# Kernel tuning notes

Measured on AMD Instinct MI355X. Metric: run time of the kernel, lower is better.

The kernel has to match this reference:

```python
import jax, jax.numpy as jnp
import numpy as np

D_MODEL = 1024
N_HEADS = 16
D_HIDDEN = 4096
BATCH = 2
N_CTX = 2048


def setup_inputs() -> dict:
    key = jax.random.key(0)
    ks = jax.random.split(key, 4)
    scale = 0.02
    x = jax.random.normal(ks[0], (BATCH, N_CTX, D_MODEL), dtype=jnp.float32)
    Wk = jax.random.normal(ks[1], (D_MODEL, D_MODEL), dtype=jnp.float32) * scale
    bk = jnp.zeros((D_MODEL,), dtype=jnp.float32)
    Wv = jax.random.normal(ks[2], (D_MODEL, D_HIDDEN), dtype=jnp.float32) * scale
    bv = jnp.zeros((D_HIDDEN,), dtype=jnp.float32)
    Wf = jax.random.normal(ks[3], (D_HIDDEN, D_MODEL), dtype=jnp.float32) * scale
    bf = jnp.zeros((D_MODEL,), dtype=jnp.float32)
    return {"x": x, "Wk": Wk, "bk": bk, "Wv": Wv, "bv": bv, "Wf": Wf, "bf": bf}


def _split_heads(t, n_heads):
    # [..., S, D] -> [..., H, S, D/H]
    B, S, D = t.shape
    return t.reshape(B, S, n_heads, D // n_heads).transpose(0, 2, 1, 3)


def reference(x, Wk, bk, Wv, bv, Wf, bf):
    B, S, D = x.shape
    H = N_HEADS
    # Q is raw x split into heads (no query projection in this module)
    Q = _split_heads(x, H)                  # [B,H,S,dk]
    K = _split_heads(x @ Wk + bk, H)        # [B,H,S,dk]
    V = _split_heads(x @ Wv + bv, H)        # [B,H,S,dv]
    # additive causal mask: 0 on/below diagonal, -inf strictly above
    causal = jnp.tril(jnp.ones((S, S), dtype=bool))
    mask = jnp.where(causal, 0.0, -jnp.inf).astype(x.dtype)
    # NOTE: no 1/sqrt(d) scaling, faithful to the original
    scores = jnp.einsum("bhqd,bhkd->bhqk", Q, K) + mask
    attn = jax.nn.softmax(scores, axis=-1)
    o = jnp.einsum("bhqk,bhkd->bhqd", attn, V)   # [B,H,S,dv]
    o = o.transpose(0, 2, 1, 3).reshape(B, S, -1)  # [B,S,d_hidden]
    return x + jax.nn.gelu(o, approximate=False) @ Wf + bf
```

## Files before the change

kernel.cpp:

```cpp
#include <hip/hip_runtime.h>
#include <math.h>

typedef unsigned short u16;
typedef __attribute__((ext_vector_type(8))) short bf16x8;
typedef __attribute__((ext_vector_type(4))) float f32x4;

__device__ __forceinline__ float b2f(u16 u) {
    union { unsigned int i; float f; } v; v.i = ((unsigned int)u) << 16; return v.f;
}
__device__ __forceinline__ u16 f2b(float f) {
    union { float f; unsigned int i; } v; v.f = f;
    unsigned int r = v.i + 0x7FFFu + ((v.i >> 16) & 1u);
    return (u16)(r >> 16);
}
__device__ __forceinline__ float gelu_exact(float v) {
    return 0.5f * v * (1.0f + erff(v * 0.70710678118654752f));
}

__device__ __forceinline__ void load_lds16(const u16* gp, u16* lp) {
    __builtin_amdgcn_global_load_lds(
        (const __attribute__((address_space(1))) void*)gp,
        (__attribute__((address_space(3))) void*)lp,
        16, 0, 0);
}

__global__ __launch_bounds__(256) void convert_f2b(const float* __restrict__ in,
                                                   u16* __restrict__ out) {
    const int idx = blockIdx.x * 256 + threadIdx.x;
    float4 v = ((const float4*)in)[idx];
    ushort4 u; u.x = f2b(v.x); u.y = f2b(v.y); u.z = f2b(v.z); u.w = f2b(v.w);
    ((ushort4*)out)[idx] = u;
}

__global__ __launch_bounds__(256) void transpose_w(const float* __restrict__ W,
                                                   u16* __restrict__ Wt, int N, int K) {
    __shared__ float t[32][33];
    const int tid = threadIdx.x;
    const int k0 = blockIdx.y * 32, n0 = blockIdx.x * 32;
    const int c = tid & 31, r = tid >> 5;
    #pragma unroll
    for (int p = 0; p < 4; p++)
        t[r + p * 8][c] = W[(size_t)(k0 + r + p * 8) * N + n0 + c];
    __syncthreads();
    #pragma unroll
    for (int p = 0; p < 4; p++)
        Wt[(size_t)(n0 + r + p * 8) * K + k0 + c] = f2b(t[c][r + p * 8]);
}

__global__ __launch_bounds__(256) void transpose_v(const u16* __restrict__ V,
                                                   u16* __restrict__ Vt) {
    __shared__ u16 t[32][36];
    const int tid = threadIdx.x;
    const int bb = blockIdx.z;
    const int s0 = blockIdx.y * 32, c0 = blockIdx.x * 32;
    const int c = tid & 31, r = tid >> 5;
    #pragma unroll
    for (int p = 0; p < 4; p++)
        t[r + p * 8][c] = V[((size_t)(bb * 2048 + s0 + r + p * 8) << 12) + c0 + c];
    __syncthreads();
    #pragma unroll
    for (int p = 0; p < 4; p++)
        Vt[((size_t)(bb * 4096 + c0 + r + p * 8) << 11) + s0 + c] = t[c][r + p * 8];
}

template <int EPI>
__global__ __launch_bounds__(256) void mfma_gemm(
    const u16* __restrict__ A, const u16* __restrict__ Bt,
    const float* __restrict__ bias, const float* __restrict__ resid,
    void* __restrict__ Cv, int M, int N, int K)
{
    __shared__ u16 As[64 * 64];
    __shared__ u16 Bs[128 * 64];

    const int tid = threadIdx.x;
    const int w = tid >> 6, lane = tid & 63;
    const int m16 = lane & 15, quad = lane >> 4;
    const int wm = w >> 1, wn = w & 1;
    const int row0 = blockIdx.y * 64, col0 = blockIdx.x * 128;
    const int lr = lane >> 3, lc = lane & 7;
    const int sw8 = (lc ^ (lr & 7)) * 8;

    f32x4 acc[2][4];
    #pragma unroll
    for (int i = 0; i < 2; i++)
        #pragma unroll
        for (int j = 0; j < 4; j++) acc[i][j] = (f32x4){0.f, 0.f, 0.f, 0.f};

    for (int k0 = 0; k0 < K; k0 += 64) {
        __syncthreads();
        #pragma unroll
        for (int c2 = 0; c2 < 2; c2++)
            load_lds16(A + (size_t)(row0 + c2 * 32 + w * 8 + lr) * K + k0 + sw8,
                       &As[(c2 * 32 + w * 8) * 64]);
        #pragma unroll
        for (int c2 = 0; c2 < 4; c2++)
            load_lds16(Bt + (size_t)(col0 + c2 * 32 + w * 8 + lr) * K + k0 + sw8,
                       &Bs[(c2 * 32 + w * 8) * 64]);
        __syncthreads();

        bf16x8 af[2][2], bfr[4][2];
        #pragma unroll
        for (int mt = 0; mt < 2; mt++)
            #pragma unroll
            for (int ks = 0; ks < 2; ks++)
                af[mt][ks] = *(const bf16x8*)&As[(wm * 32 + mt * 16 + m16) * 64 +
                                                 (((ks * 4 + quad) ^ (m16 & 7)) * 8)];
        #pragma unroll
        for (int nt = 0; nt < 4; nt++)
            #pragma unroll
            for (int ks = 0; ks < 2; ks++)
                bfr[nt][ks] = *(const bf16x8*)&Bs[(wn * 64 + nt * 16 + m16) * 64 +
                                                  (((ks * 4 + quad) ^ (m16 & 7)) * 8)];

        #pragma unroll
        for (int ks = 0; ks < 2; ks++)
            #pragma unroll
            for (int mt = 0; mt < 2; mt++)
                #pragma unroll
                for (int nt = 0; nt < 4; nt++)
                    acc[mt][nt] = __builtin_amdgcn_mfma_f32_16x16x32_bf16(af[mt][ks], bfr[nt][ks], acc[mt][nt], 0, 0, 0);
    }

    #pragma unroll
    for (int mt = 0; mt < 2; mt++) {
        #pragma unroll
        for (int nt = 0; nt < 4; nt++) {
            const int c = col0 + wn * 64 + nt * 16 + m16;
            const float bc = bias[c];
            #pragma unroll
            for (int reg = 0; reg < 4; reg++) {
                const int r = row0 + wm * 32 + mt * 16 + quad * 4 + reg;
                float v = acc[mt][nt][reg] + bc;
                if (EPI == 1) {
                    v += resid[(size_t)r * N + c];
                    ((float*)Cv)[(size_t)r * N + c] = v;
                } else {
                    ((u16*)Cv)[(size_t)r * N + c] = f2b(v);
                }
            }
        }
    }
}

__global__ __launch_bounds__(256) void attn_kernel(
    const float* __restrict__ X,
    const u16*  __restrict__ Kb,
    const u16*  __restrict__ Vt,
    u16* __restrict__ O,
    int B, int S)
{
    const int DM = 1024, DH = 4096;
    __shared__ u16 Qs[64 * 64];
    __shared__ u16 Ks[64 * 64];
    __shared__ u16 Ps[64 * 64];
    __shared__ u16 Vts[256 * 64];

    const int tid = threadIdx.x;
    const int w = tid >> 6, lane = tid & 63;
    const int m16 = lane & 15, quad = lane >> 4;
    const int lr = lane >> 3, lc = lane & 7;
    const int sw8 = (lc ^ (lr & 7)) * 8;
    const int b = blockIdx.z, h = blockIdx.y;
    const int qt = (S / 64 - 1) - blockIdx.x;
    const int q0 = qt * 64;
    const size_t baseRow = (size_t)b * S;

    #pragma unroll
    for (int pass = 0; pass < 2; pass++) {
        const int row = pass * 32 + w * 8 + lr;
        const float* src = X + (baseRow + q0 + row) * DM + h * 64 + sw8;
        float4 v0 = ((const float4*)src)[0];
        float4 v1 = ((const float4*)src)[1];
        bf16x8 u;
        u[0] = (short)f2b(v0.x); u[1] = (short)f2b(v0.y); u[2] = (short)f2b(v0.z); u[3] = (short)f2b(v0.w);
        u[4] = (short)f2b(v1.x); u[5] = (short)f2b(v1.y); u[6] = (short)f2b(v1.z); u[7] = (short)f2b(v1.w);
        *(bf16x8*)&Qs[(pass * 32 + w * 8) * 64 + lane * 8] = u;
    }

    f32x4 o_acc[16];
    #pragma unroll
    for (int i = 0; i < 16; i++) o_acc[i] = (f32x4){0.f, 0.f, 0.f, 0.f};
    f32x4 lacc = (f32x4){0.f, 0.f, 0.f, 0.f};

    bf16x8 onesf;
    {
        const short one = (m16 == 0) ? (short)0x3F80 : (short)0;
        #pragma unroll
        for (int i = 0; i < 8; i++) onesf[i] = one;
    }

    const int nch = qt + 1;
    for (int ch = 0; ch < nch; ch++) {
        const int k0 = ch * 64;
        __syncthreads();

        #pragma unroll
        for (int pass = 0; pass < 2; pass++) {
            const int row = pass * 32 + w * 8 + lr;
            *(bf16x8*)&Ks[(pass * 32 + w * 8) * 64 + lane * 8] =
                *(const bf16x8*)(Kb + (baseRow + k0 + row) * DM + h * 64 + sw8);
        }
        #pragma unroll
        for (int pass = 0; pass < 8; pass++) {
            const int row = pass * 32 + w * 8 + lr;
            *(bf16x8*)&Vts[(pass * 32 + w * 8) * 64 + lane * 8] =
                *(const bf16x8*)(Vt + (((size_t)((b * 16 + h) * 256 + row)) << 11) + k0 + sw8);
        }
        __syncthreads();

        bf16x8 aq[2];
        #pragma unroll
        for (int ks = 0; ks < 2; ks++)
            aq[ks] = *(const bf16x8*)&Qs[(w * 16 + m16) * 64 + (((ks * 4 + quad) ^ (m16 & 7)) * 8)];
        f32x4 sf[4];
        #pragma unroll
        for (int nt = 0; nt < 4; nt++) {
            f32x4 acc = (f32x4){0.f, 0.f, 0.f, 0.f};
            #pragma unroll
            for (int ks = 0; ks < 2; ks++) {
                bf16x8 bk8 = *(const bf16x8*)&Ks[(nt * 16 + m16) * 64 + (((ks * 4 + quad) ^ (m16 & 7)) * 8)];
                acc = __builtin_amdgcn_mfma_f32_16x16x32_bf16(aq[ks], bk8, acc, 0, 0, 0);
            }
            sf[nt] = acc;
        }

        const int qg = q0 + w * 16 + quad * 4;
        #pragma unroll
        for (int nt = 0; nt < 4; nt++) {
            const int kg = k0 + nt * 16 + m16;
            #pragma unroll
            for (int reg = 0; reg < 4; reg++) {
                const float p = (kg <= qg + reg) ? __expf(sf[nt][reg] - 20.f) : 0.f;
                const int srow = w * 16 + quad * 4 + reg;
                Ps[srow * 64 + (((nt * 2 + (m16 >> 3)) ^ (srow & 7)) * 8) + (m16 & 7)] = f2b(p);
            }
        }

        bf16x8 pa[2];
        #pragma unroll
        for (int ks = 0; ks < 2; ks++)
            pa[ks] = *(const bf16x8*)&Ps[(w * 16 + m16) * 64 + (((ks * 4 + quad) ^ (m16 & 7)) * 8)];
        #pragma unroll
        for (int ks = 0; ks < 2; ks++)
            lacc = __builtin_amdgcn_mfma_f32_16x16x32_bf16(pa[ks], onesf, lacc, 0, 0, 0);
        #pragma unroll
        for (int nt2 = 0; nt2 < 16; nt2++) {
            f32x4 acc = o_acc[nt2];
            #pragma unroll
            for (int ks = 0; ks < 2; ks++) {
                bf16x8 bv8 = *(const bf16x8*)&Vts[(nt2 * 16 + m16) * 64 + (((ks * 4 + quad) ^ (m16 & 7)) * 8)];
                acc = __builtin_amdgcn_mfma_f32_16x16x32_bf16(pa[ks], bv8, acc, 0, 0, 0);
            }
            o_acc[nt2] = acc;
        }
    }

    #pragma unroll
    for (int reg = 0; reg < 4; reg++) {
        const float l = __shfl(lacc[reg], quad * 16);
        const float invl = 1.0f / l;
        u16* orow = O + (baseRow + q0 + w * 16 + quad * 4 + reg) * DH + h * 256 + m16;
        #pragma unroll
        for (int nt2 = 0; nt2 < 16; nt2++)
            orow[nt2 * 16] = f2b(gelu_exact(o_acc[nt2][reg] * invl));
    }
}

extern "C" void kernel_launch(void* const* d_in, const int* in_sizes, int n_in,
                              void* d_out, int out_size, void* d_ws, size_t ws_size,
                              hipStream_t stream)
{
    const float* x   = (const float*)d_in[0];
    const float* Wk  = (const float*)d_in[1];
    const float* bk  = (const float*)d_in[2];
    const float* Wv  = (const float*)d_in[3];
    const float* bv  = (const float*)d_in[4];
    const float* Wf  = (const float*)d_in[5];
    const float* bfb = (const float*)d_in[6];
    float* out = (float*)d_out;

    const int Bsz = 2, S = 2048, DM = 1024, DH = 4096;
    const int M = Bsz * S;
    const size_t MB = 1024 * 1024;

    u16* xb   = (u16*)d_ws;
    u16* Wkt  = xb   + 4 * MB;
    u16* Wvt  = Wkt  + 1 * MB;
    u16* Wft  = Wvt  + 4 * MB;
    u16* Kbuf = Wft  + 4 * MB;
    u16* Vbuf = Kbuf + 4 * MB;
    u16* Vt   = Vbuf + 16 * MB;
    u16* Obuf = Vbuf;

    dim3 blk(256);

    convert_f2b<<<dim3(M * DM / 1024), blk, 0, stream>>>(x, xb);
    transpose_w<<<dim3(DM / 32, DM / 32), blk, 0, stream>>>(Wk, Wkt, DM, DM);
    transpose_w<<<dim3(DH / 32, DM / 32), blk, 0, stream>>>(Wv, Wvt, DH, DM);
    transpose_w<<<dim3(DM / 32, DH / 32), blk, 0, stream>>>(Wf, Wft, DM, DH);

    mfma_gemm<0><<<dim3(DM / 128, M / 64), blk, 0, stream>>>(xb, Wkt, bk, nullptr, Kbuf, M, DM, DM);
    mfma_gemm<0><<<dim3(DH / 128, M / 64), blk, 0, stream>>>(xb, Wvt, bv, nullptr, Vbuf, M, DH, DM);
    transpose_v<<<dim3(DH / 32, S / 32, Bsz), blk, 0, stream>>>(Vbuf, Vt);
    attn_kernel<<<dim3(S / 64, 16, Bsz), blk, 0, stream>>>(x, Kbuf, Vt, Obuf, Bsz, S);
    mfma_gemm<1><<<dim3(DM / 128, M / 64), blk, 0, stream>>>(Obuf, Wft, bfb, x, out, M, DM, DH);
}
```

Before: 403.5 us.

## Fuse V transpose into GEMM epilogue and prefetch K/V tiles in attention

The V projection GEMM now writes its output directly in the transposed per-head layout the attention kernel reads, which removes the separate transpose_v kernel and its round trip through a 16M-element buffer. In the attention kernel, Q fragments are loaded straight from global memory into registers instead of going through shared memory. The next chunk's K and V tiles are also loaded into registers while the current chunk computes, then stored to LDS after a barrier. This adds register pressure from ten extra bf16x8 values per thread, and the epilogue's scattered 8-byte stores into the transposed layout may coalesce poorly.

```diff
diff --git a/kernel.cpp b/kernel.cpp
--- a/kernel.cpp
+++ b/kernel.cpp
@@ -45,22 +45,6 @@
     #pragma unroll
     for (int p = 0; p < 4; p++)
         Wt[(size_t)(n0 + r + p * 8) * K + k0 + c] = f2b(t[c][r + p * 8]);
-}
-
-__global__ __launch_bounds__(256) void transpose_v(const u16* __restrict__ V,
-                                                   u16* __restrict__ Vt) {
-    __shared__ u16 t[32][36];
-    const int tid = threadIdx.x;
-    const int bb = blockIdx.z;
-    const int s0 = blockIdx.y * 32, c0 = blockIdx.x * 32;
-    const int c = tid & 31, r = tid >> 5;
-    #pragma unroll
-    for (int p = 0; p < 4; p++)
-        t[r + p * 8][c] = V[((size_t)(bb * 2048 + s0 + r + p * 8) << 12) + c0 + c];
-    __syncthreads();
-    #pragma unroll
-    for (int p = 0; p < 4; p++)
-        Vt[((size_t)(bb * 4096 + c0 + r + p * 8) << 11) + s0 + c] = t[c][r + p * 8];
 }
 
 template <int EPI>
@@ -127,15 +111,27 @@
         for (int nt = 0; nt < 4; nt++) {
             const int c = col0 + wn * 64 + nt * 16 + m16;
             const float bc = bias[c];
-            #pragma unroll
-            for (int reg = 0; reg < 4; reg++) {
-                const int r = row0 + wm * 32 + mt * 16 + quad * 4 + reg;
-                float v = acc[mt][nt][reg] + bc;
-                if (EPI == 1) {
-                    v += resid[(size_t)r * N + c];
-                    ((float*)Cv)[(size_t)r * N + c] = v;
-                } else {
-                    ((u16*)Cv)[(size_t)r * N + c] = f2b(v);
+            if (EPI == 2) {
+                const int r0 = row0 + wm * 32 + mt * 16 + quad * 4;
+                const int bb = r0 >> 11, s = r0 & 2047;
+                const int h = c >> 8, dv = c & 255;
+                ushort4 w4;
+                w4.x = f2b(acc[mt][nt][0] + bc);
+                w4.y = f2b(acc[mt][nt][1] + bc);
+                w4.z = f2b(acc[mt][nt][2] + bc);
+                w4.w = f2b(acc[mt][nt][3] + bc);
+                *(ushort4*)((u16*)Cv + (((size_t)((bb * 16 + h) * 256 + dv)) << 11) + s) = w4;
+            } else {
+                #pragma unroll
+                for (int reg = 0; reg < 4; reg++) {
+                    const int r = row0 + wm * 32 + mt * 16 + quad * 4 + reg;
+                    float v = acc[mt][nt][reg] + bc;
+                    if (EPI == 1) {
+                        v += resid[(size_t)r * N + c];
+                        ((float*)Cv)[(size_t)r * N + c] = v;
+                    } else {
+                        ((u16*)Cv)[(size_t)r * N + c] = f2b(v);
+                    }
                 }
             }
         }
@@ -150,7 +146,6 @@
     int B, int S)
 {
     const int DM = 1024, DH = 4096;
-    __shared__ u16 Qs[64 * 64];
     __shared__ u16 Ks[64 * 64];
     __shared__ u16 Ps[64 * 64];
     __shared__ u16 Vts[256 * 64];
@@ -164,17 +159,20 @@
     const int qt = (S / 64 - 1) - blockIdx.x;
     const int q0 = qt * 64;
     const size_t baseRow = (size_t)b * S;
-
-    #pragma unroll
-    for (int pass = 0; pass < 2; pass++) {
-        const int row = pass * 32 + w * 8 + lr;
-        const float* src = X + (baseRow + q0 + row) * DM + h * 64 + sw8;
-        float4 v0 = ((const float4*)src)[0];
-        float4 v1 = ((const float4*)src)[1];
-        bf16x8 u;
-        u[0] = (short)f2b(v0.x); u[1] = (short)f2b(v0.y); u[2] = (short)f2b(v0.z); u[3] = (short)f2b(v0.w);
-        u[4] = (short)f2b(v1.x); u[5] = (short)f2b(v1.y); u[6] = (short)f2b(v1.z); u[7] = (short)f2b(v1.w);
-        *(bf16x8*)&Qs[(pass * 32 + w * 8) * 64 + lane * 8] = u;
+    const size_t vhead = ((size_t)(b * 16 + h) * 256) << 11;
+
+    bf16x8 aq[2];
+    {
+        const float* qsrc = X + (baseRow + q0 + w * 16 + m16) * DM + h * 64;
+        #pragma unroll
+        for (int ks = 0; ks < 2; ks++) {
+            float4 v0 = *(const float4*)(qsrc + ks * 32 + quad * 8);
+            float4 v1 = *(const float4*)(qsrc + ks * 32 + quad * 8 + 4);
+            bf16x8 u;
+            u[0] = (short)f2b(v0.x); u[1] = (short)f2b(v0.y); u[2] = (short)f2b(v0.z); u[3] = (short)f2b(v0.w);
+            u[4] = (short)f2b(v1.x); u[5] = (short)f2b(v1.y); u[6] = (short)f2b(v1.z); u[7] = (short)f2b(v1.w);
+            aq[ks] = u;
+        }
     }
 
     f32x4 o_acc[16];
@@ -189,29 +187,36 @@
         for (int i = 0; i < 8; i++) onesf[i] = one;
     }
 
+    bf16x8 kreg[2], vreg[8];
+
+    #pragma unroll
+    for (int p = 0; p < 2; p++)
+        kreg[p] = *(const bf16x8*)(Kb + (baseRow + p * 32 + w * 8 + lr) * DM + h * 64 + sw8);
+    #pragma unroll
+    for (int p = 0; p < 8; p++)
+        vreg[p] = *(const bf16x8*)(Vt + vhead + (((size_t)(p * 32 + w * 8 + lr)) << 11) + sw8);
+    #pragma unroll
+    for (int p = 0; p < 2; p++)
+        *(bf16x8*)&Ks[(p * 32 + w * 8) * 64 + lane * 8] = kreg[p];
+    #pragma unroll
+    for (int p = 0; p < 8; p++)
+        *(bf16x8*)&Vts[(p * 32 + w * 8) * 64 + lane * 8] = vreg[p];
+    __syncthreads();
+
     const int nch = qt + 1;
     for (int ch = 0; ch < nch; ch++) {
         const int k0 = ch * 64;
-        __syncthreads();
-
-        #pragma unroll
-        for (int pass = 0; pass < 2; pass++) {
-            const int row = pass * 32 + w * 8 + lr;
-            *(bf16x8*)&Ks[(pass * 32 + w * 8) * 64 + lane * 8] =
-                *(const bf16x8*)(Kb + (baseRow + k0 + row) * DM + h * 64 + sw8);
-        }
-        #pragma unroll
-        for (int pass = 0; pass < 8; pass++) {
-            const int row = pass * 32 + w * 8 + lr;
-            *(bf16x8*)&Vts[(pass * 32 + w * 8) * 64 + lane * 8] =
-                *(const bf16x8*)(Vt + (((size_t)((b * 16 + h) * 256 + row)) << 11) + k0 + sw8);
-        }
-        __syncthreads();
-
-        bf16x8 aq[2];
-        #pragma unroll
-        for (int ks = 0; ks < 2; ks++)
-            aq[ks] = *(const bf16x8*)&Qs[(w * 16 + m16) * 64 + (((ks * 4 + quad) ^ (m16 & 7)) * 8)];
+
+        if (ch + 1 < nch) {
+            const int kn = k0 + 64;
+            #pragma unroll
+            for (int p = 0; p < 2; p++)
+                kreg[p] = *(const bf16x8*)(Kb + (baseRow + kn + p * 32 + w * 8 + lr) * DM + h * 64 + sw8);
+            #pragma unroll
+            for (int p = 0; p < 8; p++)
+                vreg[p] = *(const bf16x8*)(Vt + vhead + (((size_t)(p * 32 + w * 8 + lr)) << 11) + kn + sw8);
+        }
+
         f32x4 sf[4];
         #pragma unroll
         for (int nt = 0; nt < 4; nt++) {
@@ -252,6 +257,17 @@
                 acc = __builtin_amdgcn_mfma_f32_16x16x32_bf16(pa[ks], bv8, acc, 0, 0, 0);
             }
             o_acc[nt2] = acc;
+        }
+
+        __syncthreads();
+        if (ch + 1 < nch) {
+            #pragma unroll
+            for (int p = 0; p < 2; p++)
+                *(bf16x8*)&Ks[(p * 32 + w * 8) * 64 + lane * 8] = kreg[p];
+            #pragma unroll
+            for (int p = 0; p < 8; p++)
+                *(bf16x8*)&Vts[(p * 32 + w * 8) * 64 + lane * 8] = vreg[p];
+            __syncthreads();
         }
     }
 
@@ -288,9 +304,8 @@
     u16* Wvt  = Wkt  + 1 * MB;
     u16* Wft  = Wvt  + 4 * MB;
     u16* Kbuf = Wft  + 4 * MB;
-    u16* Vbuf = Kbuf + 4 * MB;
-    u16* Vt   = Vbuf + 16 * MB;
-    u16* Obuf = Vbuf;
+    u16* Vt   = Kbuf + 4 * MB;
+    u16* Obuf = Vt   + 16 * MB;
 
     dim3 blk(256);
 
@@ -300,8 +315,7 @@
     transpose_w<<<dim3(DM / 32, DH / 32), blk, 0, stream>>>(Wf, Wft, DM, DH);
 
     mfma_gemm<0><<<dim3(DM / 128, M / 64), blk, 0, stream>>>(xb, Wkt, bk, nullptr, Kbuf, M, DM, DM);
-    mfma_gemm<0><<<dim3(DH / 128, M / 64), blk, 0, stream>>>(xb, Wvt, bv, nullptr, Vbuf, M, DH, DM);
-    transpose_v<<<dim3(DH / 32, S / 32, Bsz), blk, 0, stream>>>(Vbuf, Vt);
+    mfma_gemm<2><<<dim3(DH / 128, M / 64), blk, 0, stream>>>(xb, Wvt, bv, nullptr, Vt, M, DH, DM);
     attn_kernel<<<dim3(S / 64, 16, Bsz), blk, 0, stream>>>(x, Kbuf, Vt, Obuf, Bsz, S);
     mfma_gemm<1><<<dim3(DM / 128, M / 64), blk, 0, stream>>>(Obuf, Wft, bfb, x, out, M, DM, DH);
 }
```

Result: faster. 388.7 us (-3.7%).
